# Optimization experiments

Measured on AMD Instinct MI355X. Metric: run time of the kernel, lower is better.

The kernel has to match this reference:

```python
import jax, jax.numpy as jnp
import numpy as np
import math

INPUT_SIZE = 1024
HIDDEN_SIZE = 1024
RANK = 256
BATCH = 32
SEQ = 512


def setup_inputs() -> dict:
    key = jax.random.key(0)
    k_x, k_a, k_b, k_c = jax.random.split(key, 4)
    stdv = 1.0 / math.sqrt(HIDDEN_SIZE)
    x = jax.random.normal(k_x, (BATCH, SEQ, INPUT_SIZE), dtype=jnp.float32)
    a = jax.random.uniform(k_a, (HIDDEN_SIZE, RANK * 4), minval=-stdv, maxval=stdv, dtype=jnp.float32)
    b = jax.random.uniform(k_b, (INPUT_SIZE, RANK * 4), minval=-stdv, maxval=stdv, dtype=jnp.float32)
    ct = jax.random.uniform(k_c, (RANK * 4, HIDDEN_SIZE), minval=-stdv, maxval=stdv, dtype=jnp.float32)
    return {"x": x, "a": a, "b": b, "ct": ct}


def reference(x, a, b, ct):
    B, S, _ = x.shape
    H = a.shape[0]
    R = a.shape[1] // 4
    ct3 = ct.reshape(4, R, H)  # (4, R, H)
    # Precompute input projection for all timesteps: (B, S, 4R)
    xb = jnp.einsum('bsi,ir->bsr', x, b)

    def step(carry, xb_t):
        h, c = carry
        g = (h @ a) * xb_t                      # (B, 4R)
        g = jnp.einsum('bkr,krh->bkh', g.reshape(B, 4, R), ct3)  # (B, 4, H)
        f_t = jax.nn.sigmoid(g[:, 0])
        i_t = jax.nn.sigmoid(g[:, 1])
        g_t = jnp.tanh(g[:, 2])
        o_t = jax.nn.sigmoid(g[:, 3])
        c = f_t * c + i_t * g_t
        h = o_t * jnp.tanh(c)
        return (h, c), h

    h0 = jnp.zeros((B, H), dtype=x.dtype)
    c0 = jnp.zeros((B, H), dtype=x.dtype)
    (h_t, c_t), hs = jax.lax.scan(step, (h0, c0), jnp.swapaxes(xb, 0, 1))
    hidden_seq = jnp.swapaxes(hs, 0, 1)  # (B, S, H)
    return hidden_seq, (h_t, c_t)
```

## Files before the change

### kernel.cpp

```cpp
#include <hip/hip_runtime.h>
#include <math.h>

#define NTHR 512

__device__ __forceinline__ void st_uc(float* p, float v) {
    asm volatile("global_store_dword %0, %1, off sc0 sc1" :: "v"(p), "v"(v) : "memory");
}

__global__ void init_kernel(float* bufs, unsigned* flags) {
    int i = blockIdx.x * blockDim.x + threadIdx.x;
    if (i < 65536) bufs[i] = 0.0f;
    if (i < 4096) flags[i] = 0u;
}

__global__ __launch_bounds__(256) void xb_gemm(const float* __restrict__ X,
                                               const float* __restrict__ Bw,
                                               float* __restrict__ XB) {
    __shared__ float xs[16][132];
    __shared__ float bs[16][132];
    const int bm = blockIdx.x >> 3;
    const int bn = blockIdx.x & 7;
    const int m0 = bm * 128, n0 = bn * 128;
    const int tid = threadIdx.x;
    const int tx = tid & 15, ty = tid >> 4;
    float acc[8][8];
#pragma unroll
    for (int i = 0; i < 8; ++i)
#pragma unroll
        for (int j = 0; j < 8; ++j) acc[i][j] = 0.f;

    for (int k0 = 0; k0 < 1024; k0 += 16) {
#pragma unroll
        for (int p = 0; p < 2; ++p) {
            int f = tid + p * 256;
            int m = f >> 2, kq = f & 3;
            float4 v = *(const float4*)&X[(size_t)(m0 + m) * 1024 + k0 + kq * 4];
            xs[kq * 4 + 0][m] = v.x; xs[kq * 4 + 1][m] = v.y;
            xs[kq * 4 + 2][m] = v.z; xs[kq * 4 + 3][m] = v.w;
        }
#pragma unroll
        for (int p = 0; p < 2; ++p) {
            int f = tid + p * 256;
            int k = f >> 5, n = (f & 31) * 4;
            float4 v = *(const float4*)&Bw[(size_t)(k0 + k) * 1024 + n0 + n];
            *(float4*)&bs[k][n] = v;
        }
        __syncthreads();
#pragma unroll
        for (int k = 0; k < 16; ++k) {
            float xv[8], bv[8];
            *(float4*)&xv[0] = *(const float4*)&xs[k][ty * 8];
            *(float4*)&xv[4] = *(const float4*)&xs[k][ty * 8 + 4];
            *(float4*)&bv[0] = *(const float4*)&bs[k][tx * 8];
            *(float4*)&bv[4] = *(const float4*)&bs[k][tx * 8 + 4];
#pragma unroll
            for (int i = 0; i < 8; ++i)
#pragma unroll
                for (int j = 0; j < 8; ++j) acc[i][j] += xv[i] * bv[j];
        }
        __syncthreads();
    }
#pragma unroll
    for (int i = 0; i < 8; ++i)
#pragma unroll
        for (int j = 0; j < 8; j += 4) {
            float4 v = make_float4(acc[i][j], acc[i][j + 1], acc[i][j + 2], acc[i][j + 3]);
            *(float4*)&XB[(size_t)(m0 + ty * 8 + i) * 1024 + n0 + tx * 8 + j] = v;
        }
}

__device__ __forceinline__ void group_barrier(unsigned* gf, int sub, int tid, unsigned bar) {
    asm volatile("s_waitcnt vmcnt(0)" ::: "memory");
    __syncthreads();
    if (tid == 0) {
        bool last = false;
        unsigned a = __hip_atomic_fetch_add(gf + (sub << 5), 1u, __ATOMIC_RELAXED, __HIP_MEMORY_SCOPE_AGENT);
        if (a == bar * 8u - 1u) {
            unsigned b = __hip_atomic_fetch_add(gf + 256, 1u, __ATOMIC_RELAXED, __HIP_MEMORY_SCOPE_AGENT);
            if (b == bar * 8u - 1u) {
                __hip_atomic_store(gf + 288, bar, __ATOMIC_RELAXED, __HIP_MEMORY_SCOPE_AGENT);
                last = true;
            }
        }
        if (!last) {
            while (__hip_atomic_load(gf + 288, __ATOMIC_RELAXED, __HIP_MEMORY_SCOPE_AGENT) < bar)
                __builtin_amdgcn_s_sleep(1);
        }
    }
    __syncthreads();
}

__global__ __launch_bounds__(NTHR, 1) void scan_kernel(
    const float* __restrict__ A, const float* __restrict__ CTm,
    float* __restrict__ XBH, float* __restrict__ h_buf, float* __restrict__ g_buf,
    float* __restrict__ ht_out, float* __restrict__ ct_out, unsigned* flags) {
    extern __shared__ float lds[];
    float4* a_l  = (float4*)lds;
    float4* ct_l = a_l + 4096;
    float4* hg_s = ct_l + 4096;

    const int wg = blockIdx.x;
    const int bg = wg >> 6;
    const int sg = wg & 63;
    const int c0wg = sg * 16;
    const int tid = threadIdx.x;
    unsigned* gf = flags + (bg << 10);
    const int sub = sg >> 3;

    {
        const int c = tid & 15, i0 = tid >> 4;
        float* al_f  = (float*)a_l;
        float* ctl_f = (float*)ct_l;
        for (int i = i0; i < 1024; i += 32) {
            int p4  = (i >> 2) ^ ((i >> 6) & 7);
            int idx = (c << 10) + (p4 << 2) + (i & 3);
            al_f[idx]  = A[(size_t)i * 1024 + c0wg + c];
            ctl_f[idx] = CTm[(size_t)i * 1024 + c0wg + c];
        }
    }

    const int bp = tid >> 7;
    const int cp = (tid >> 4) & 7;
    const int q  = tid & 15;
    const int qs = q & 7;
    const int fb = q << 4;
    const int s  = q & 3;
    const int gt_i = q >> 2;
    const int bl = 2 * bp + (s & 1);
    const int cl = 2 * cp + (s >> 1);
    const int bglob = bg * 8 + bl;
    const int cglob = c0wg + cl;

    const float* hsrc = h_buf + (size_t)(bg * 8) * 1024;
    const float* gsrc = g_buf + (size_t)(bg * 8) * 1024;

    float creg = 0.f;
    __syncthreads();

    for (int t = 0; t < 512; ++t) {
        {
            const float4* s4 = (const float4*)hsrc;
            float4 v0, v1, v2, v3;
            asm volatile("global_load_dwordx4 %0, %1, off sc0 sc1" : "=v"(v0) : "v"(s4 + tid) : "memory");
            asm volatile("global_load_dwordx4 %0, %1, off sc0 sc1" : "=v"(v1) : "v"(s4 + 512 + tid) : "memory");
            asm volatile("global_load_dwordx4 %0, %1, off sc0 sc1" : "=v"(v2) : "v"(s4 + 1024 + tid) : "memory");
            asm volatile("global_load_dwordx4 %0, %1, off sc0 sc1" : "=v"(v3) : "v"(s4 + 1536 + tid) : "memory");
            asm volatile("s_waitcnt vmcnt(0)" ::: "memory");
            __builtin_amdgcn_sched_barrier(0);
            int u0 = tid, u1 = tid + 512, u2 = tid + 1024, u3 = tid + 1536;
            hg_s[(u0 & ~255) | ((u0 & 255) ^ ((u0 >> 4) & 7))] = v0;
            hg_s[(u1 & ~255) | ((u1 & 255) ^ ((u1 >> 4) & 7))] = v1;
            hg_s[(u2 & ~255) | ((u2 & 255) ^ ((u2 >> 4) & 7))] = v2;
            hg_s[(u3 & ~255) | ((u3 & 255) ^ ((u3 >> 4) & 7))] = v3;
            __syncthreads();
        }
        {
            const float4* ac0 = a_l + (cp << 9);
            const float4* ac1 = ac0 + 256;
            const float4* hr0 = hg_s + (bp << 9);
            const float4* hr1 = hr0 + 256;
            float a00 = 0.f, a01 = 0.f, a10 = 0.f, a11 = 0.f;
#pragma unroll
            for (int ii = 0; ii < 16; ++ii) {
                int p = (fb + ii) ^ qs;
                float4 av0 = ac0[p], av1 = ac1[p], hv0 = hr0[p], hv1 = hr1[p];
                a00 += av0.x * hv0.x + av0.y * hv0.y + av0.z * hv0.z + av0.w * hv0.w;
                a01 += av0.x * hv1.x + av0.y * hv1.y + av0.z * hv1.z + av0.w * hv1.w;
                a10 += av1.x * hv0.x + av1.y * hv0.y + av1.z * hv0.z + av1.w * hv0.w;
                a11 += av1.x * hv1.x + av1.y * hv1.y + av1.z * hv1.z + av1.w * hv1.w;
            }
            a00 += __shfl_xor(a00, 1); a00 += __shfl_xor(a00, 2);
            a01 += __shfl_xor(a01, 1); a01 += __shfl_xor(a01, 2);
            a10 += __shfl_xor(a10, 1); a10 += __shfl_xor(a10, 2);
            a11 += __shfl_xor(a11, 1); a11 += __shfl_xor(a11, 2);
            float pown = (q & 2) ? ((q & 1) ? a11 : a10) : ((q & 1) ? a01 : a00);
            pown += __shfl_xor(pown, 4);
            pown += __shfl_xor(pown, 8);
            if (q < 4) {
                float xbv = XBH[((size_t)bglob * 512 + t) * 1024 + cglob];
                st_uc(g_buf + (size_t)bglob * 1024 + cglob, pown * xbv);
            }
        }
        group_barrier(gf, sub, tid, 2 * (unsigned)t + 1u);

        {
            const float4* s4 = (const float4*)gsrc;
            float4 v0, v1, v2, v3;
            asm volatile("global_load_dwordx4 %0, %1, off sc0 sc1" : "=v"(v0) : "v"(s4 + tid) : "memory");
            asm volatile("global_load_dwordx4 %0, %1, off sc0 sc1" : "=v"(v1) : "v"(s4 + 512 + tid) : "memory");
            asm volatile("global_load_dwordx4 %0, %1, off sc0 sc1" : "=v"(v2) : "v"(s4 + 1024 + tid) : "memory");
            asm volatile("global_load_dwordx4 %0, %1, off sc0 sc1" : "=v"(v3) : "v"(s4 + 1536 + tid) : "memory");
            asm volatile("s_waitcnt vmcnt(0)" ::: "memory");
            __builtin_amdgcn_sched_barrier(0);
            int u0 = tid, u1 = tid + 512, u2 = tid + 1024, u3 = tid + 1536;
            hg_s[(u0 & ~255) | ((u0 & 255) ^ ((u0 >> 4) & 7))] = v0;
            hg_s[(u1 & ~255) | ((u1 & 255) ^ ((u1 >> 4) & 7))] = v1;
            hg_s[(u2 & ~255) | ((u2 & 255) ^ ((u2 >> 4) & 7))] = v2;
            hg_s[(u3 & ~255) | ((u3 & 255) ^ ((u3 >> 4) & 7))] = v3;
            __syncthreads();
        }
        {
            const float4* cc0 = ct_l + (cp << 9);
            const float4* cc1 = cc0 + 256;
            const float4* gr0 = hg_s + (bp << 9);
            const float4* gr1 = gr0 + 256;
            float a00 = 0.f, a01 = 0.f, a10 = 0.f, a11 = 0.f;
#pragma unroll
            for (int ii = 0; ii < 16; ++ii) {
                int p = (fb + ii) ^ qs;
                float4 cv0 = cc0[p], cv1 = cc1[p], gv0 = gr0[p], gv1 = gr1[p];
                a00 += cv0.x * gv0.x + cv0.y * gv0.y + cv0.z * gv0.z + cv0.w * gv0.w;
                a01 += cv0.x * gv1.x + cv0.y * gv1.y + cv0.z * gv1.z + cv0.w * gv1.w;
                a10 += cv1.x * gv0.x + cv1.y * gv0.y + cv1.z * gv0.z + cv1.w * gv0.w;
                a11 += cv1.x * gv1.x + cv1.y * gv1.y + cv1.z * gv1.z + cv1.w * gv1.w;
            }
            a00 += __shfl_xor(a00, 1); a00 += __shfl_xor(a00, 2);
            a01 += __shfl_xor(a01, 1); a01 += __shfl_xor(a01, 2);
            a10 += __shfl_xor(a10, 1); a10 += __shfl_xor(a10, 2);
            a11 += __shfl_xor(a11, 1); a11 += __shfl_xor(a11, 2);
            float pown = (q & 2) ? ((q & 1) ? a11 : a10) : ((q & 1) ? a01 : a00);
            float x = pown;
            float y = __shfl_xor(pown, 4);
            float z = __shfl_xor(pown, 8);
            float w = __shfl_xor(y, 8);
            float pf = (gt_i == 0) ? x : ((gt_i == 1) ? y : ((gt_i == 2) ? z : w));
            float pi = (gt_i == 1) ? x : ((gt_i == 0) ? y : ((gt_i == 3) ? z : w));
            float pg = (gt_i == 2) ? x : ((gt_i == 3) ? y : ((gt_i == 0) ? z : w));
            float po = (gt_i == 3) ? x : ((gt_i == 2) ? y : ((gt_i == 1) ? z : w));
            float ft = 1.f / (1.f + __expf(-pf));
            float it = 1.f / (1.f + __expf(-pi));
            float gg = tanhf(pg);
            float ot = 1.f / (1.f + __expf(-po));
            creg = ft * creg + it * gg;
            float hv = ot * tanhf(creg);
            if (q < 4) {
                st_uc(h_buf + (size_t)bglob * 1024 + cglob, hv);
                st_uc(XBH + ((size_t)bglob * 512 + t) * 1024 + cglob, hv);
                if (t == 511) {
                    st_uc(ht_out + (size_t)bglob * 1024 + cglob, hv);
                    st_uc(ct_out + (size_t)bglob * 1024 + cglob, creg);
                }
            }
        }
        group_barrier(gf, sub, tid, 2 * (unsigned)t + 2u);
    }
}

extern "C" void kernel_launch(void* const* d_in, const int* in_sizes, int n_in,
                              void* d_out, int out_size, void* d_ws, size_t ws_size,
                              hipStream_t stream) {
    const float* X   = (const float*)d_in[0];
    const float* A   = (const float*)d_in[1];
    const float* Bw  = (const float*)d_in[2];
    const float* CTm = (const float*)d_in[3];

    float* out    = (float*)d_out;
    float* XBH    = out;
    float* ht_out = out + (size_t)32 * 512 * 1024;
    float* ct_out = ht_out + 32 * 1024;

    float* h_buf = (float*)d_ws;
    float* g_buf = h_buf + 32 * 1024;
    unsigned* flags = (unsigned*)(g_buf + 32 * 1024);

    (void)hipFuncSetAttribute((const void*)scan_kernel,
                              hipFuncAttributeMaxDynamicSharedMemorySize, 163840);

    init_kernel<<<dim3(256), dim3(256), 0, stream>>>(h_buf, flags);
    xb_gemm<<<dim3(1024), dim3(256), 0, stream>>>(X, Bw, XBH);
    scan_kernel<<<dim3(256), dim3(NTHR), 163840, stream>>>(A, CTm, XBH, h_buf, g_buf,
                                                           ht_out, ct_out, flags);
}
```

Before: 5.404 ms.

## Restructure per-step matvec into 8x8 register tiles with lane-parallel K reduction

The per-timestep dot products are remapped so each thread holds an 8x8 batch-by-column tile, with the K dimension spread across the 64 lanes of a wave. Results are combined with a butterfly shuffle reduction plus an LDS scratch pass, and 128 threads do the epilogue. The XB value is now loaded at the top of each step, before the h load, so its latency is off the critical path. In exchange it uses many more registers (a 64-float accumulator array), adds extra __syncthreads per phase, and leaves the LDS layout unswizzled, which may cause bank conflicts.

```diff
diff --git a/kernel.cpp b/kernel.cpp
--- a/kernel.cpp
+++ b/kernel.cpp
@@ -95,9 +95,13 @@
     float* __restrict__ XBH, float* __restrict__ h_buf, float* __restrict__ g_buf,
     float* __restrict__ ht_out, float* __restrict__ ct_out, unsigned* flags) {
     extern __shared__ float lds[];
-    float4* a_l  = (float4*)lds;
-    float4* ct_l = a_l + 4096;
-    float4* hg_s = ct_l + 4096;
+    float* a_lf  = lds;
+    float* ct_lf = lds + 16384;
+    float* hg_f  = lds + 32768;
+    float4* a_l4  = (float4*)a_lf;
+    float4* ct_l4 = (float4*)ct_lf;
+    float4* hg_4  = (float4*)hg_f;
+    float* scr = hg_f;
 
     const int wg = blockIdx.x;
     const int bg = wg >> 6;
@@ -109,140 +113,152 @@
 
     {
         const int c = tid & 15, i0 = tid >> 4;
-        float* al_f  = (float*)a_l;
-        float* ctl_f = (float*)ct_l;
         for (int i = i0; i < 1024; i += 32) {
-            int p4  = (i >> 2) ^ ((i >> 6) & 7);
-            int idx = (c << 10) + (p4 << 2) + (i & 3);
-            al_f[idx]  = A[(size_t)i * 1024 + c0wg + c];
-            ctl_f[idx] = CTm[(size_t)i * 1024 + c0wg + c];
-        }
-    }
-
-    const int bp = tid >> 7;
-    const int cp = (tid >> 4) & 7;
-    const int q  = tid & 15;
-    const int qs = q & 7;
-    const int fb = q << 4;
-    const int s  = q & 3;
-    const int gt_i = q >> 2;
-    const int bl = 2 * bp + (s & 1);
-    const int cl = 2 * cp + (s >> 1);
-    const int bglob = bg * 8 + bl;
-    const int cglob = c0wg + cl;
-
-    const float* hsrc = h_buf + (size_t)(bg * 8) * 1024;
-    const float* gsrc = g_buf + (size_t)(bg * 8) * 1024;
+            a_lf[c * 1024 + i]  = A[(size_t)i * 1024 + c0wg + c];
+            ct_lf[c * 1024 + i] = CTm[(size_t)i * 1024 + c0wg + c];
+        }
+    }
+
+    const int L  = tid & 63;
+    const int w  = tid >> 6;
+    const int Lc = L & 7;
+    const int Lb = (L >> 3) & 7;
+    const int cgA = w & 1, kqA = w >> 1;
+    const int gB  = w >> 1;
+
+    int hIdx[8], aIdx[8], gIdx[8], cIdx[8];
+#pragma unroll
+    for (int r = 0; r < 8; ++r) hIdx[r] = (r ^ Lb) * 256 + kqA * 64 + L;
+#pragma unroll
+    for (int c = 0; c < 8; ++c) aIdx[c] = (cgA * 8 + (c ^ Lc)) * 256 + kqA * 64 + L;
+#pragma unroll
+    for (int r = 0; r < 8; ++r) gIdx[r] = (r ^ Lb) * 256 + gB * 64 + L;
+#pragma unroll
+    for (int c = 0; c < 8; ++c) cIdx[c] = (cgA * 8 + (c ^ Lc)) * 256 + gB * 64 + L;
+
+    const int e_b  = tid >> 4;
+    const int e_j  = tid & 15;
+    const int e_cg = e_j >> 3;
+    const int e_slot = e_b * 8 + (e_j & 7);
+    const int e_bglob = bg * 8 + e_b;
+    const int e_col   = c0wg + e_j;
+
+    const float4* hsrc4 = (const float4*)(h_buf + (size_t)bg * 8192);
+    const float4* gsrc4 = (const float4*)(g_buf + (size_t)bg * 8192);
 
     float creg = 0.f;
+    unsigned barc = 0;
     __syncthreads();
 
     for (int t = 0; t < 512; ++t) {
-        {
-            const float4* s4 = (const float4*)hsrc;
+        float xbv = 0.f;
+        if (tid < 128) xbv = XBH[((size_t)e_bglob * 512 + t) * 1024 + e_col];
+
+        {
             float4 v0, v1, v2, v3;
-            asm volatile("global_load_dwordx4 %0, %1, off sc0 sc1" : "=v"(v0) : "v"(s4 + tid) : "memory");
-            asm volatile("global_load_dwordx4 %0, %1, off sc0 sc1" : "=v"(v1) : "v"(s4 + 512 + tid) : "memory");
-            asm volatile("global_load_dwordx4 %0, %1, off sc0 sc1" : "=v"(v2) : "v"(s4 + 1024 + tid) : "memory");
-            asm volatile("global_load_dwordx4 %0, %1, off sc0 sc1" : "=v"(v3) : "v"(s4 + 1536 + tid) : "memory");
+            asm volatile("global_load_dwordx4 %0, %1, off sc0 sc1" : "=v"(v0) : "v"(hsrc4 + tid) : "memory");
+            asm volatile("global_load_dwordx4 %0, %1, off sc0 sc1" : "=v"(v1) : "v"(hsrc4 + 512 + tid) : "memory");
+            asm volatile("global_load_dwordx4 %0, %1, off sc0 sc1" : "=v"(v2) : "v"(hsrc4 + 1024 + tid) : "memory");
+            asm volatile("global_load_dwordx4 %0, %1, off sc0 sc1" : "=v"(v3) : "v"(hsrc4 + 1536 + tid) : "memory");
             asm volatile("s_waitcnt vmcnt(0)" ::: "memory");
             __builtin_amdgcn_sched_barrier(0);
-            int u0 = tid, u1 = tid + 512, u2 = tid + 1024, u3 = tid + 1536;
-            hg_s[(u0 & ~255) | ((u0 & 255) ^ ((u0 >> 4) & 7))] = v0;
-            hg_s[(u1 & ~255) | ((u1 & 255) ^ ((u1 >> 4) & 7))] = v1;
-            hg_s[(u2 & ~255) | ((u2 & 255) ^ ((u2 >> 4) & 7))] = v2;
-            hg_s[(u3 & ~255) | ((u3 & 255) ^ ((u3 >> 4) & 7))] = v3;
+            hg_4[tid] = v0; hg_4[512 + tid] = v1; hg_4[1024 + tid] = v2; hg_4[1536 + tid] = v3;
             __syncthreads();
         }
-        {
-            const float4* ac0 = a_l + (cp << 9);
-            const float4* ac1 = ac0 + 256;
-            const float4* hr0 = hg_s + (bp << 9);
-            const float4* hr1 = hr0 + 256;
-            float a00 = 0.f, a01 = 0.f, a10 = 0.f, a11 = 0.f;
-#pragma unroll
-            for (int ii = 0; ii < 16; ++ii) {
-                int p = (fb + ii) ^ qs;
-                float4 av0 = ac0[p], av1 = ac1[p], hv0 = hr0[p], hv1 = hr1[p];
-                a00 += av0.x * hv0.x + av0.y * hv0.y + av0.z * hv0.z + av0.w * hv0.w;
-                a01 += av0.x * hv1.x + av0.y * hv1.y + av0.z * hv1.z + av0.w * hv1.w;
-                a10 += av1.x * hv0.x + av1.y * hv0.y + av1.z * hv0.z + av1.w * hv0.w;
-                a11 += av1.x * hv1.x + av1.y * hv1.y + av1.z * hv1.z + av1.w * hv1.w;
-            }
-            a00 += __shfl_xor(a00, 1); a00 += __shfl_xor(a00, 2);
-            a01 += __shfl_xor(a01, 1); a01 += __shfl_xor(a01, 2);
-            a10 += __shfl_xor(a10, 1); a10 += __shfl_xor(a10, 2);
-            a11 += __shfl_xor(a11, 1); a11 += __shfl_xor(a11, 2);
-            float pown = (q & 2) ? ((q & 1) ? a11 : a10) : ((q & 1) ? a01 : a00);
-            pown += __shfl_xor(pown, 4);
-            pown += __shfl_xor(pown, 8);
-            if (q < 4) {
-                float xbv = XBH[((size_t)bglob * 512 + t) * 1024 + cglob];
-                st_uc(g_buf + (size_t)bglob * 1024 + cglob, pown * xbv);
-            }
-        }
-        group_barrier(gf, sub, tid, 2 * (unsigned)t + 1u);
-
-        {
-            const float4* s4 = (const float4*)gsrc;
+        float v[64];
+        {
+            float4 hv[8], av[8];
+#pragma unroll
+            for (int r = 0; r < 8; ++r) hv[r] = hg_4[hIdx[r]];
+#pragma unroll
+            for (int c = 0; c < 8; ++c) av[c] = a_l4[aIdx[c]];
+#pragma unroll
+            for (int r = 0; r < 8; ++r)
+#pragma unroll
+                for (int c = 0; c < 8; ++c)
+                    v[r * 8 + c] = hv[r].x * av[c].x + hv[r].y * av[c].y
+                                 + hv[r].z * av[c].z + hv[r].w * av[c].w;
+        }
+#pragma unroll
+        for (int j = 0; j < 32; ++j) v[j] = v[2 * j] + __shfl_xor(v[2 * j + 1], 1);
+#pragma unroll
+        for (int j = 0; j < 16; ++j) v[j] = v[2 * j] + __shfl_xor(v[2 * j + 1], 2);
+#pragma unroll
+        for (int j = 0; j < 8; ++j)  v[j] = v[2 * j] + __shfl_xor(v[2 * j + 1], 4);
+#pragma unroll
+        for (int j = 0; j < 4; ++j)  v[j] = v[2 * j] + __shfl_xor(v[2 * j + 1], 8);
+#pragma unroll
+        for (int j = 0; j < 2; ++j)  v[j] = v[2 * j] + __shfl_xor(v[2 * j + 1], 16);
+        v[0] = v[0] + __shfl_xor(v[1], 32);
+
+        __syncthreads();
+        scr[w * 64 + L] = v[0];
+        __syncthreads();
+        if (tid < 128) {
+            float s = scr[(0 * 2 + e_cg) * 64 + e_slot] + scr[(1 * 2 + e_cg) * 64 + e_slot]
+                    + scr[(2 * 2 + e_cg) * 64 + e_slot] + scr[(3 * 2 + e_cg) * 64 + e_slot];
+            st_uc(g_buf + (size_t)e_bglob * 1024 + e_col, s * xbv);
+        }
+        group_barrier(gf, sub, tid, ++barc);
+
+        {
             float4 v0, v1, v2, v3;
-            asm volatile("global_load_dwordx4 %0, %1, off sc0 sc1" : "=v"(v0) : "v"(s4 + tid) : "memory");
-            asm volatile("global_load_dwordx4 %0, %1, off sc0 sc1" : "=v"(v1) : "v"(s4 + 512 + tid) : "memory");
-            asm volatile("global_load_dwordx4 %0, %1, off sc0 sc1" : "=v"(v2) : "v"(s4 + 1024 + tid) : "memory");
-            asm volatile("global_load_dwordx4 %0, %1, off sc0 sc1" : "=v"(v3) : "v"(s4 + 1536 + tid) : "memory");
+            asm volatile("global_load_dwordx4 %0, %1, off sc0 sc1" : "=v"(v0) : "v"(gsrc4 + tid) : "memory");
+            asm volatile("global_load_dwordx4 %0, %1, off sc0 sc1" : "=v"(v1) : "v"(gsrc4 + 512 + tid) : "memory");
+            asm volatile("global_load_dwordx4 %0, %1, off sc0 sc1" : "=v"(v2) : "v"(gsrc4 + 1024 + tid) : "memory");
+            asm volatile("global_load_dwordx4 %0, %1, off sc0 sc1" : "=v"(v3) : "v"(gsrc4 + 1536 + tid) : "memory");
             asm volatile("s_waitcnt vmcnt(0)" ::: "memory");
             __builtin_amdgcn_sched_barrier(0);
-            int u0 = tid, u1 = tid + 512, u2 = tid + 1024, u3 = tid + 1536;
-            hg_s[(u0 & ~255) | ((u0 & 255) ^ ((u0 >> 4) & 7))] = v0;
-            hg_s[(u1 & ~255) | ((u1 & 255) ^ ((u1 >> 4) & 7))] = v1;
-            hg_s[(u2 & ~255) | ((u2 & 255) ^ ((u2 >> 4) & 7))] = v2;
-            hg_s[(u3 & ~255) | ((u3 & 255) ^ ((u3 >> 4) & 7))] = v3;
+            hg_4[tid] = v0; hg_4[512 + tid] = v1; hg_4[1024 + tid] = v2; hg_4[1536 + tid] = v3;
             __syncthreads();
         }
         {
-            const float4* cc0 = ct_l + (cp << 9);
-            const float4* cc1 = cc0 + 256;
-            const float4* gr0 = hg_s + (bp << 9);
-            const float4* gr1 = gr0 + 256;
-            float a00 = 0.f, a01 = 0.f, a10 = 0.f, a11 = 0.f;
-#pragma unroll
-            for (int ii = 0; ii < 16; ++ii) {
-                int p = (fb + ii) ^ qs;
-                float4 cv0 = cc0[p], cv1 = cc1[p], gv0 = gr0[p], gv1 = gr1[p];
-                a00 += cv0.x * gv0.x + cv0.y * gv0.y + cv0.z * gv0.z + cv0.w * gv0.w;
-                a01 += cv0.x * gv1.x + cv0.y * gv1.y + cv0.z * gv1.z + cv0.w * gv1.w;
-                a10 += cv1.x * gv0.x + cv1.y * gv0.y + cv1.z * gv0.z + cv1.w * gv0.w;
-                a11 += cv1.x * gv1.x + cv1.y * gv1.y + cv1.z * gv1.z + cv1.w * gv1.w;
-            }
-            a00 += __shfl_xor(a00, 1); a00 += __shfl_xor(a00, 2);
-            a01 += __shfl_xor(a01, 1); a01 += __shfl_xor(a01, 2);
-            a10 += __shfl_xor(a10, 1); a10 += __shfl_xor(a10, 2);
-            a11 += __shfl_xor(a11, 1); a11 += __shfl_xor(a11, 2);
-            float pown = (q & 2) ? ((q & 1) ? a11 : a10) : ((q & 1) ? a01 : a00);
-            float x = pown;
-            float y = __shfl_xor(pown, 4);
-            float z = __shfl_xor(pown, 8);
-            float w = __shfl_xor(y, 8);
-            float pf = (gt_i == 0) ? x : ((gt_i == 1) ? y : ((gt_i == 2) ? z : w));
-            float pi = (gt_i == 1) ? x : ((gt_i == 0) ? y : ((gt_i == 3) ? z : w));
-            float pg = (gt_i == 2) ? x : ((gt_i == 3) ? y : ((gt_i == 0) ? z : w));
-            float po = (gt_i == 3) ? x : ((gt_i == 2) ? y : ((gt_i == 1) ? z : w));
+            float4 gv[8], cv[8];
+#pragma unroll
+            for (int r = 0; r < 8; ++r) gv[r] = hg_4[gIdx[r]];
+#pragma unroll
+            for (int c = 0; c < 8; ++c) cv[c] = ct_l4[cIdx[c]];
+#pragma unroll
+            for (int r = 0; r < 8; ++r)
+#pragma unroll
+                for (int c = 0; c < 8; ++c)
+                    v[r * 8 + c] = gv[r].x * cv[c].x + gv[r].y * cv[c].y
+                                 + gv[r].z * cv[c].z + gv[r].w * cv[c].w;
+        }
+#pragma unroll
+        for (int j = 0; j < 32; ++j) v[j] = v[2 * j] + __shfl_xor(v[2 * j + 1], 1);
+#pragma unroll
+        for (int j = 0; j < 16; ++j) v[j] = v[2 * j] + __shfl_xor(v[2 * j + 1], 2);
+#pragma unroll
+        for (int j = 0; j < 8; ++j)  v[j] = v[2 * j] + __shfl_xor(v[2 * j + 1], 4);
+#pragma unroll
+        for (int j = 0; j < 4; ++j)  v[j] = v[2 * j] + __shfl_xor(v[2 * j + 1], 8);
+#pragma unroll
+        for (int j = 0; j < 2; ++j)  v[j] = v[2 * j] + __shfl_xor(v[2 * j + 1], 16);
+        v[0] = v[0] + __shfl_xor(v[1], 32);
+
+        __syncthreads();
+        scr[w * 64 + L] = v[0];
+        __syncthreads();
+        if (tid < 128) {
+            float pf = scr[(0 * 2 + e_cg) * 64 + e_slot];
+            float pi = scr[(1 * 2 + e_cg) * 64 + e_slot];
+            float pg = scr[(2 * 2 + e_cg) * 64 + e_slot];
+            float po = scr[(3 * 2 + e_cg) * 64 + e_slot];
             float ft = 1.f / (1.f + __expf(-pf));
             float it = 1.f / (1.f + __expf(-pi));
-            float gg = tanhf(pg);
+            float gt = tanhf(pg);
             float ot = 1.f / (1.f + __expf(-po));
-            creg = ft * creg + it * gg;
-            float hv = ot * tanhf(creg);
-            if (q < 4) {
-                st_uc(h_buf + (size_t)bglob * 1024 + cglob, hv);
-                st_uc(XBH + ((size_t)bglob * 512 + t) * 1024 + cglob, hv);
-                if (t == 511) {
-                    st_uc(ht_out + (size_t)bglob * 1024 + cglob, hv);
-                    st_uc(ct_out + (size_t)bglob * 1024 + cglob, creg);
-                }
+            creg = ft * creg + it * gt;
+            float hv2 = ot * tanhf(creg);
+            st_uc(h_buf + (size_t)e_bglob * 1024 + e_col, hv2);
+            st_uc(XBH + ((size_t)e_bglob * 512 + t) * 1024 + e_col, hv2);
+            if (t == 511) {
+                st_uc(ht_out + (size_t)e_bglob * 1024 + e_col, hv2);
+                st_uc(ct_out + (size_t)e_bglob * 1024 + e_col, creg);
             }
         }
-        group_barrier(gf, sub, tid, 2 * (unsigned)t + 2u);
+        group_barrier(gf, sub, tid, ++barc);
     }
 }
 
```

Result: no change. 5.307 ms (-1.8%).
